# Optimization experiments

Hardware: AMD Instinct MI355X
Metric: run time of the kernel (lower is better)

## Reference

```python
import jax, jax.numpy as jnp
import numpy as np

T, E = 16384, 1024   # frames, feature dim (WavLM-Large)
M, K = 8, 512        # number of kmeans models, clusters per model


def setup_inputs() -> dict:
    key = jax.random.key(0)
    k1, k2, k3 = jax.random.split(key, 3)
    emb = jax.random.normal(k1, (1, T, E), dtype=jnp.float32)
    centroids = jax.random.normal(k2, (M, K, E), dtype=jnp.float32)
    # per-frame random kmeans model choice (stride=1): replaces random.randint in the loop
    model_idx = jax.random.randint(k3, (T,), 0, M, dtype=jnp.int32)
    return {"emb": emb, "centroids": centroids, "model_idx": model_idx}


def reference(emb, centroids, model_idx):
    # emb: [1,T,E], centroids: [M,K,E], model_idx: [T] in [0,M)
    x = emb[0]  # [T,E]
    # squared euclidean distance from every frame to every centroid of every model
    # (argmin over squared dist == argmin over cdist)
    x_sq = jnp.sum(x * x, axis=-1)                      # [T]
    c_sq = jnp.sum(centroids * centroids, axis=-1)      # [M,K]
    dots = jnp.einsum('te,mke->tmk', x, centroids)      # [T,M,K]
    d_all = x_sq[:, None, None] - 2.0 * dots + c_sq[None, :, :]  # [T,M,K]
    # select the randomly chosen model's distances per frame
    d = jnp.take_along_axis(d_all, model_idx[:, None, None].astype(jnp.int32), axis=1)[:, 0, :]  # [T,K]
    codes = jnp.argmin(d, axis=-1)                      # [T]
    # embedding lookup: the quantizer's emb maps cluster id -> centroid vector
    out = centroids[model_idx, codes]                   # [T,E]
    return out[None]  # [1,T,E]
```

## Files before the change

kernel.cpp:

```cpp
#include <hip/hip_runtime.h>


#define T_FRAMES 16384
#define E_DIM    1024
#define M_MODELS 8
#define K_CLUST  512

#define FPB 32
#define NCH 8

typedef __bf16 bf16x8 __attribute__((ext_vector_type(8)));
typedef float  floatx16 __attribute__((ext_vector_type(16)));

__device__ __forceinline__ bf16x8 cvt8(const float4 a, const float4 b) {
  bf16x8 h;
  h[0] = (__bf16)a.x; h[1] = (__bf16)a.y; h[2] = (__bf16)a.z; h[3] = (__bf16)a.w;
  h[4] = (__bf16)b.x; h[5] = (__bf16)b.y; h[6] = (__bf16)b.z; h[7] = (__bf16)b.w;
  return h;
}

__global__ __launch_bounds__(256) void k_cvt(const float* __restrict__ cent,
                                             float* __restrict__ out,
                                             double* __restrict__ csq64) {
  const int b = blockIdx.x;
  const int m = b >> 6;
  const int cg = (b >> 2) & 15;
  const int q = b & 3;
  const int tid = threadIdx.x;
  const int ci = tid & 31;
  const int t8 = tid >> 5;
  const int gk0 = q * 32 + t8 * 4;
  const int B32 = (m * 16 + cg) * 32;
  const float* src = cent + ((size_t)(m * K_CLUST + cg * 32 + ci)) * E_DIM;
  double ss = 0.0;
#pragma unroll
  for (int j = 0; j < 4; ++j) {
    const int gk = gk0 + j;
    const float4 a = *(const float4*)(src + gk * 8);
    const float4 bb = *(const float4*)(src + gk * 8 + 4);
    ss += (double)a.x * a.x + (double)a.y * a.y + (double)a.z * a.z +
          (double)a.w * a.w + (double)bb.x * bb.x + (double)bb.y * bb.y +
          (double)bb.z * bb.z + (double)bb.w * bb.w;
    const size_t foff = (size_t)(B32 + (gk >> 2)) * 1024 + 512 +
                        ((gk & 3) * 32 + ci) * 4;
    *(bf16x8*)(out + foff) = cvt8(a, bb);
  }
  __shared__ double csq_l[32][8];
  csq_l[ci][t8] = ss;
  __syncthreads();
  if (tid < 32) {
    double s = 0.0;
#pragma unroll
    for (int t = 0; t < 8; ++t) s += csq_l[tid][t];
    atomicAdd(&csq64[m * K_CLUST + cg * 32 + tid], s);
  }
}

__global__ __launch_bounds__(256) void k_hist(const int* __restrict__ midx,
                                              int* __restrict__ hist,
                                              double* __restrict__ csq64) {
  __shared__ int h[M_MODELS * 33];
  const int tid = threadIdx.x;
  if (tid < 64) csq64[blockIdx.x * 64 + tid] = 0.0;
  for (int i = tid; i < M_MODELS * 33; i += 256) h[i] = 0;
  __syncthreads();
  const int m = midx[blockIdx.x * 256 + tid];
  atomicAdd(&h[m * 33 + (tid & 31)], 1);
  __syncthreads();
  if (tid < M_MODELS) {
    int s = 0;
    for (int j = 0; j < 32; ++j) s += h[tid * 33 + j];
    hist[blockIdx.x * M_MODELS + tid] = s;
  }
}

__global__ __launch_bounds__(256) void k_scatter(const int* __restrict__ midx,
                                                 const int* __restrict__ hist,
                                                 int* __restrict__ order,
                                                 int* __restrict__ offs) {
  __shared__ int h2[64 * M_MODELS];
  __shared__ int cur[M_MODELS];
  const int tid = threadIdx.x;
  h2[tid] = hist[tid];
  h2[tid + 256] = hist[tid + 256];
  __syncthreads();
  if (tid < M_MODELS) {
    int tot_before = 0;
    for (int mp = 0; mp < tid; ++mp)
      for (int b = 0; b < 64; ++b) tot_before += h2[b * M_MODELS + mp];
    int prior = 0;
    for (int b = 0; b < (int)blockIdx.x; ++b) prior += h2[b * M_MODELS + tid];
    cur[tid] = tot_before + prior;
  }
  if (blockIdx.x == 0 && tid <= M_MODELS) {
    int o = 0;
    for (int mp = 0; mp < tid; ++mp)
      for (int b = 0; b < 64; ++b) o += h2[b * M_MODELS + mp];
    offs[tid] = o;
  }
  __syncthreads();
  const int f = blockIdx.x * 256 + tid;
  const int pos = atomicAdd(&cur[midx[f]], 1);
  order[pos] = f;
}

__global__ __launch_bounds__(512, 4) void k_dist(const float* __restrict__ emb,
                                                 const float* __restrict__ cent,
                                                 const double* __restrict__ csq64,
                                                 const int* __restrict__ order,
                                                 const int* __restrict__ offs,
                                                 float* __restrict__ out) {
  const int m = blockIdx.x;
  const int o0 = offs[m];
  const int cnt = offs[m + 1] - o0;
  const int start = blockIdx.y * FPB;
  if (start >= cnt) return;
  const int nvalid = min(FPB, cnt - start);

  __shared__ __align__(16) __bf16 A_l[2 * 16 * FPB * 8];
  __shared__ int rows_l[FPB];
  __shared__ float wmin_s[8][FPB];
  __shared__ int wcol_s[8][FPB];
  __shared__ float gmin_s[FPB];
  __shared__ int cnt_s[FPB];
  __shared__ int cand_s[FPB][32];

  const int tid = threadIdx.x;
  const int l = tid & 63;
  const int w = tid >> 6;
  const int ln = l & 31;
  const int lh = l >> 5;

  if (tid < FPB) rows_l[tid] = order[o0 + start + min(tid, nvalid - 1)];
  __syncthreads();

  const int s_row = tid & 31;
  const int s_g = tid >> 5;
  const float4* emb4 = (const float4*)emb;
  const size_t arow4 = (size_t)rows_l[s_row] * (E_DIM / 4);

  float4 pa[2];
  pa[0] = emb4[arow4 + s_g * 2 + 0];
  pa[1] = emb4[arow4 + s_g * 2 + 1];
  *(bf16x8*)(A_l + ((s_g)*FPB + s_row) * 8) = cvt8(pa[0], pa[1]);

  const char* bbase[2];
#pragma unroll
  for (int ct = 0; ct < 2; ++ct) {
    const int cg = w * 2 + ct;
    bbase[ct] = (const char*)out + (size_t)(m * 16 + cg) * 131072 + 2048 + l * 16;
  }
#define LOADB(ct, kb) (*(const bf16x8*)(bbase[ct] + (((kb) >> 1) << 12) + (((kb) & 1) << 10)))

  bf16x8 bR[4][2];
#pragma unroll
  for (int d = 0; d < 4; ++d)
#pragma unroll
    for (int ct = 0; ct < 2; ++ct) bR[d][ct] = LOADB(ct, d);

  floatx16 acc[2] = {};

  for (int c = 0; c < NCH; ++c) {
    __syncthreads();
    const int buf = (c & 1) * 16;
    if (c + 1 < NCH) {
      pa[0] = emb4[arow4 + (c + 1) * 32 + s_g * 2 + 0];
      pa[1] = emb4[arow4 + (c + 1) * 32 + s_g * 2 + 1];
    }
#pragma unroll
    for (int jj = 0; jj < 8; ++jj) {
      const int kb = c * 8 + jj;
      const int p = kb & 3;
      const bf16x8 a0 = *(const bf16x8*)(A_l + ((buf + jj * 2 + lh) * FPB + ln) * 8);
      acc[0] = __builtin_amdgcn_mfma_f32_32x32x16_bf16(a0, bR[p][0], acc[0], 0, 0, 0);
      acc[1] = __builtin_amdgcn_mfma_f32_32x32x16_bf16(a0, bR[p][1], acc[1], 0, 0, 0);
      if (kb + 4 < 64) {
        bR[p][0] = LOADB(0, kb + 4);
        bR[p][1] = LOADB(1, kb + 4);
      }
    }
    if (c + 1 < NCH) {
      const int nbuf = ((c + 1) & 1) * 16;
      *(bf16x8*)(A_l + ((nbuf + s_g) * FPB + s_row) * 8) = cvt8(pa[0], pa[1]);
    }
  }
#undef LOADB

  float cs[2];
#pragma unroll
  for (int ct = 0; ct < 2; ++ct)
    cs[ct] = (float)csq64[m * K_CLUST + w * 64 + ct * 32 + ln];

#pragma unroll
  for (int r = 0; r < 16; ++r) {
    const int fr = (r & 3) + 8 * (r >> 2) + 4 * lh;
    float bm = cs[0] - 2.0f * acc[0][r];
    int bc = w * 64 + ln;
    {
      const float s = cs[1] - 2.0f * acc[1][r];
      if (s < bm) { bm = s; bc = w * 64 + 32 + ln; }
    }
#pragma unroll
    for (int sh = 1; sh <= 16; sh <<= 1) {
      const float om = __shfl_xor(bm, sh, 64);
      const int oc = __shfl_xor(bc, sh, 64);
      if (om < bm || (om == bm && oc < bc)) { bm = om; bc = oc; }
    }
    if (ln == 0) { wmin_s[w][fr] = bm; wcol_s[w][fr] = bc; }
  }
  __syncthreads();

  if (tid < FPB) {
    float g = wmin_s[0][tid];
    int gc = wcol_s[0][tid];
#pragma unroll
    for (int w2 = 1; w2 < 8; ++w2) {
      const float v = wmin_s[w2][tid];
      const int vc = wcol_s[w2][tid];
      if (v < g || (v == g && vc < gc)) { g = v; gc = vc; }
    }
    gmin_s[tid] = g;
    cnt_s[tid] = 0;
  }
  __syncthreads();

#pragma unroll
  for (int r = 0; r < 16; ++r) {
    const int fr = (r & 3) + 8 * (r >> 2) + 4 * lh;
    const float thr = gmin_s[fr] + 3.0f;
#pragma unroll
    for (int ct = 0; ct < 2; ++ct) {
      const float s = cs[ct] - 2.0f * acc[ct][r];
      if (s < thr) {
        const int ix = atomicAdd(&cnt_s[fr], 1);
        if (ix < 32) cand_s[fr][ix] = w * 64 + ct * 32 + ln;
      }
    }
  }
  __syncthreads();

  for (int i = 0; i < 4; ++i) {
    const int f = w * 4 + i;
    const int t = rows_l[f];
    const int n = min(cnt_s[f], 32);
    int code;
    if (n == 1) {
      code = cand_s[f][0];
    } else {
      float4 xv[4];
#pragma unroll
      for (int q = 0; q < 4; ++q) xv[q] = emb4[(size_t)t * (E_DIM / 4) + q * 64 + l];
      double bd = 1e300;
      int bi = 1 << 30;
      for (int j = 0; j < n; ++j) {
        const int cc = cand_s[f][j];
        const float4* crow4 = (const float4*)(cent + ((size_t)(m * K_CLUST + cc)) * E_DIM);
        double s = 0.0;
#pragma unroll
        for (int q = 0; q < 4; ++q) {
          const float4 cv = crow4[q * 64 + l];
          s += (double)xv[q].x * cv.x + (double)xv[q].y * cv.y +
               (double)xv[q].z * cv.z + (double)xv[q].w * cv.w;
        }
#pragma unroll
        for (int sh = 32; sh >= 1; sh >>= 1) s += __shfl_xor(s, sh, 64);
        const double d = csq64[m * K_CLUST + cc] - 2.0 * s;
        if (d < bd || (d == bd && cc < bi)) { bd = d; bi = cc; }
      }
      code = bi;
    }
    if (t >= 4096) {
      const float4* crow = (const float4*)(cent + ((size_t)(m * K_CLUST + code)) * E_DIM);
      float4* drow = (float4*)(out + (size_t)t * E_DIM);
#pragma unroll
      for (int q = 0; q < 4; ++q) drow[q * 64 + l] = crow[q * 64 + l];
    } else if (l == 0) {
      *(int*)(out + (size_t)t * E_DIM) = code;
    }
  }
}

__global__ __launch_bounds__(256) void k_gather(const float* __restrict__ cent,
                                                const int* __restrict__ midx,
                                                float* __restrict__ out) {
  const int t = blockIdx.x * 4 + (threadIdx.x >> 6);
  const int l = threadIdx.x & 63;
  float* drow = out + (size_t)t * E_DIM;
  const int code = *(const int*)drow;
  const int m = midx[t];
  const float4* src = (const float4*)(cent + ((size_t)(m * K_CLUST + code)) * E_DIM);
  float4* dst = (float4*)drow;
#pragma unroll
  for (int q = 0; q < 4; ++q) dst[q * 64 + l] = src[q * 64 + l];
}

extern "C" void kernel_launch(void* const* d_in, const int* in_sizes, int n_in,
                              void* d_out, int out_size, void* d_ws, size_t ws_size,
                              hipStream_t stream) {
  const float* emb = (const float*)d_in[0];
  const float* cent = (const float*)d_in[1];
  const int* midx = (const int*)d_in[2];
  float* out = (float*)d_out;

  char* ws = (char*)d_ws;
  double* csq64 = (double*)(ws + 0);
  int* hist = (int*)(ws + 32768);
  int* offs = (int*)(ws + 34816);
  int* order = (int*)(ws + 34880);

  hipLaunchKernelGGL(k_hist, dim3(64), dim3(256), 0, stream, midx, hist, csq64);
  hipLaunchKernelGGL(k_scatter, dim3(64), dim3(256), 0, stream, midx, hist, order, offs);
  hipLaunchKernelGGL(k_cvt, dim3(512), dim3(256), 0, stream, cent, out, csq64);
  hipLaunchKernelGGL(k_dist, dim3(M_MODELS, 80), dim3(512), 0, stream,
                     emb, cent, csq64, order, offs, out);
  hipLaunchKernelGGL(k_gather, dim3(4096 / 4), dim3(256), 0, stream,
                     cent, midx, out);
}
```

Baseline: 202.4 us.

## Double frames per block in distance kernel and move candidate resolve to separate kernel

Raises the distance kernel's frame tile from 32 to 64 rows. Each loaded centroid B fragment now feeds two MFMA row tiles, which halves B traffic per frame, and the grid shrinks accordingly. The fp64 candidate refinement and the centroid copy-out move out of the distance kernel into a new resolve kernel that runs over all frames. The distance kernel now only writes the candidate count and list into the output rows. This trades a lower occupancy bound and an extra global round trip for less B reloading and a lighter tail in the matmul kernel.

```diff
diff --git a/kernel.cpp b/kernel.cpp
--- a/kernel.cpp
+++ b/kernel.cpp
@@ -6,7 +6,7 @@
 #define M_MODELS 8
 #define K_CLUST  512
 
-#define FPB 32
+#define FPB 64
 #define NCH 8
 
 typedef __bf16 bf16x8 __attribute__((ext_vector_type(8)));
@@ -104,7 +104,7 @@
   order[pos] = f;
 }
 
-__global__ __launch_bounds__(512, 4) void k_dist(const float* __restrict__ emb,
+__global__ __launch_bounds__(512, 2) void k_dist(const float* __restrict__ emb,
                                                  const float* __restrict__ cent,
                                                  const double* __restrict__ csq64,
                                                  const int* __restrict__ order,
@@ -134,15 +134,16 @@
   if (tid < FPB) rows_l[tid] = order[o0 + start + min(tid, nvalid - 1)];
   __syncthreads();
 
-  const int s_row = tid & 31;
-  const int s_g = tid >> 5;
+  const int s_row = tid & 63;
+  const int s_g = tid >> 6;
   const float4* emb4 = (const float4*)emb;
   const size_t arow4 = (size_t)rows_l[s_row] * (E_DIM / 4);
 
-  float4 pa[2];
-  pa[0] = emb4[arow4 + s_g * 2 + 0];
-  pa[1] = emb4[arow4 + s_g * 2 + 1];
-  *(bf16x8*)(A_l + ((s_g)*FPB + s_row) * 8) = cvt8(pa[0], pa[1]);
+  float4 pa[4];
+#pragma unroll
+  for (int j = 0; j < 4; ++j) pa[j] = emb4[arow4 + s_g * 4 + j];
+  *(bf16x8*)(A_l + ((s_g * 2 + 0) * FPB + s_row) * 8) = cvt8(pa[0], pa[1]);
+  *(bf16x8*)(A_l + ((s_g * 2 + 1) * FPB + s_row) * 8) = cvt8(pa[2], pa[3]);
 
   const char* bbase[2];
 #pragma unroll
@@ -158,22 +159,25 @@
 #pragma unroll
     for (int ct = 0; ct < 2; ++ct) bR[d][ct] = LOADB(ct, d);
 
-  floatx16 acc[2] = {};
+  floatx16 acc[2][2] = {};
 
   for (int c = 0; c < NCH; ++c) {
     __syncthreads();
     const int buf = (c & 1) * 16;
     if (c + 1 < NCH) {
-      pa[0] = emb4[arow4 + (c + 1) * 32 + s_g * 2 + 0];
-      pa[1] = emb4[arow4 + (c + 1) * 32 + s_g * 2 + 1];
+#pragma unroll
+      for (int j = 0; j < 4; ++j) pa[j] = emb4[arow4 + (c + 1) * 32 + s_g * 4 + j];
     }
 #pragma unroll
     for (int jj = 0; jj < 8; ++jj) {
       const int kb = c * 8 + jj;
       const int p = kb & 3;
       const bf16x8 a0 = *(const bf16x8*)(A_l + ((buf + jj * 2 + lh) * FPB + ln) * 8);
-      acc[0] = __builtin_amdgcn_mfma_f32_32x32x16_bf16(a0, bR[p][0], acc[0], 0, 0, 0);
-      acc[1] = __builtin_amdgcn_mfma_f32_32x32x16_bf16(a0, bR[p][1], acc[1], 0, 0, 0);
+      const bf16x8 a1 = *(const bf16x8*)(A_l + ((buf + jj * 2 + lh) * FPB + 32 + ln) * 8);
+      acc[0][0] = __builtin_amdgcn_mfma_f32_32x32x16_bf16(a0, bR[p][0], acc[0][0], 0, 0, 0);
+      acc[0][1] = __builtin_amdgcn_mfma_f32_32x32x16_bf16(a0, bR[p][1], acc[0][1], 0, 0, 0);
+      acc[1][0] = __builtin_amdgcn_mfma_f32_32x32x16_bf16(a1, bR[p][0], acc[1][0], 0, 0, 0);
+      acc[1][1] = __builtin_amdgcn_mfma_f32_32x32x16_bf16(a1, bR[p][1], acc[1][1], 0, 0, 0);
       if (kb + 4 < 64) {
         bR[p][0] = LOADB(0, kb + 4);
         bR[p][1] = LOADB(1, kb + 4);
@@ -181,7 +185,8 @@
     }
     if (c + 1 < NCH) {
       const int nbuf = ((c + 1) & 1) * 16;
-      *(bf16x8*)(A_l + ((nbuf + s_g) * FPB + s_row) * 8) = cvt8(pa[0], pa[1]);
+      *(bf16x8*)(A_l + ((nbuf + s_g * 2 + 0) * FPB + s_row) * 8) = cvt8(pa[0], pa[1]);
+      *(bf16x8*)(A_l + ((nbuf + s_g * 2 + 1) * FPB + s_row) * 8) = cvt8(pa[2], pa[3]);
     }
   }
 #undef LOADB
@@ -192,102 +197,106 @@
     cs[ct] = (float)csq64[m * K_CLUST + w * 64 + ct * 32 + ln];
 
 #pragma unroll
-  for (int r = 0; r < 16; ++r) {
-    const int fr = (r & 3) + 8 * (r >> 2) + 4 * lh;
-    float bm = cs[0] - 2.0f * acc[0][r];
-    int bc = w * 64 + ln;
-    {
-      const float s = cs[1] - 2.0f * acc[1][r];
-      if (s < bm) { bm = s; bc = w * 64 + 32 + ln; }
-    }
-#pragma unroll
-    for (int sh = 1; sh <= 16; sh <<= 1) {
-      const float om = __shfl_xor(bm, sh, 64);
-      const int oc = __shfl_xor(bc, sh, 64);
-      if (om < bm || (om == bm && oc < bc)) { bm = om; bc = oc; }
-    }
-    if (ln == 0) { wmin_s[w][fr] = bm; wcol_s[w][fr] = bc; }
-  }
-  __syncthreads();
-
-  if (tid < FPB) {
-    float g = wmin_s[0][tid];
-    int gc = wcol_s[0][tid];
+  for (int rt = 0; rt < 2; ++rt) {
+#pragma unroll
+    for (int r = 0; r < 16; ++r) {
+      const int fr = rt * 32 + (r & 3) + 8 * (r >> 2) + 4 * lh;
+      float bm = cs[0] - 2.0f * acc[rt][0][r];
+      int bc = w * 64 + ln;
+      {
+        const float s = cs[1] - 2.0f * acc[rt][1][r];
+        if (s < bm) { bm = s; bc = w * 64 + 32 + ln; }
+      }
+#pragma unroll
+      for (int sh = 1; sh <= 16; sh <<= 1) {
+        const float om = __shfl_xor(bm, sh, 64);
+        const int oc = __shfl_xor(bc, sh, 64);
+        if (om < bm || (om == bm && oc < bc)) { bm = om; bc = oc; }
+      }
+      if (ln == 0) { wmin_s[w][fr] = bm; wcol_s[w][fr] = bc; }
+    }
+  }
+  __syncthreads();
+
+  for (int f0 = tid; f0 < FPB; f0 += 512) {
+    float g = wmin_s[0][f0];
+    int gc = wcol_s[0][f0];
 #pragma unroll
     for (int w2 = 1; w2 < 8; ++w2) {
-      const float v = wmin_s[w2][tid];
-      const int vc = wcol_s[w2][tid];
+      const float v = wmin_s[w2][f0];
+      const int vc = wcol_s[w2][f0];
       if (v < g || (v == g && vc < gc)) { g = v; gc = vc; }
     }
-    gmin_s[tid] = g;
-    cnt_s[tid] = 0;
-  }
-  __syncthreads();
-
-#pragma unroll
-  for (int r = 0; r < 16; ++r) {
-    const int fr = (r & 3) + 8 * (r >> 2) + 4 * lh;
-    const float thr = gmin_s[fr] + 3.0f;
-#pragma unroll
-    for (int ct = 0; ct < 2; ++ct) {
-      const float s = cs[ct] - 2.0f * acc[ct][r];
-      if (s < thr) {
-        const int ix = atomicAdd(&cnt_s[fr], 1);
-        if (ix < 32) cand_s[fr][ix] = w * 64 + ct * 32 + ln;
-      }
-    }
-  }
-  __syncthreads();
-
-  for (int i = 0; i < 4; ++i) {
-    const int f = w * 4 + i;
+    gmin_s[f0] = g;
+    cnt_s[f0] = 0;
+  }
+  __syncthreads();
+
+#pragma unroll
+  for (int rt = 0; rt < 2; ++rt) {
+#pragma unroll
+    for (int r = 0; r < 16; ++r) {
+      const int fr = rt * 32 + (r & 3) + 8 * (r >> 2) + 4 * lh;
+      const float thr = gmin_s[fr] + 3.0f;
+#pragma unroll
+      for (int ct = 0; ct < 2; ++ct) {
+        const float s = cs[ct] - 2.0f * acc[rt][ct][r];
+        if (s < thr) {
+          const int ix = atomicAdd(&cnt_s[fr], 1);
+          if (ix < 32) cand_s[fr][ix] = w * 64 + ct * 32 + ln;
+        }
+      }
+    }
+  }
+  __syncthreads();
+
+  for (int i = 0; i < 8; ++i) {
+    const int f = w * 8 + i;
+    if (f >= nvalid) continue;
     const int t = rows_l[f];
     const int n = min(cnt_s[f], 32);
-    int code;
-    if (n == 1) {
-      code = cand_s[f][0];
-    } else {
-      float4 xv[4];
-#pragma unroll
-      for (int q = 0; q < 4; ++q) xv[q] = emb4[(size_t)t * (E_DIM / 4) + q * 64 + l];
-      double bd = 1e300;
-      int bi = 1 << 30;
-      for (int j = 0; j < n; ++j) {
-        const int cc = cand_s[f][j];
-        const float4* crow4 = (const float4*)(cent + ((size_t)(m * K_CLUST + cc)) * E_DIM);
-        double s = 0.0;
-#pragma unroll
-        for (int q = 0; q < 4; ++q) {
-          const float4 cv = crow4[q * 64 + l];
-          s += (double)xv[q].x * cv.x + (double)xv[q].y * cv.y +
-               (double)xv[q].z * cv.z + (double)xv[q].w * cv.w;
-        }
-#pragma unroll
-        for (int sh = 32; sh >= 1; sh >>= 1) s += __shfl_xor(s, sh, 64);
-        const double d = csq64[m * K_CLUST + cc] - 2.0 * s;
-        if (d < bd || (d == bd && cc < bi)) { bd = d; bi = cc; }
-      }
-      code = bi;
-    }
-    if (t >= 4096) {
-      const float4* crow = (const float4*)(cent + ((size_t)(m * K_CLUST + code)) * E_DIM);
-      float4* drow = (float4*)(out + (size_t)t * E_DIM);
-#pragma unroll
-      for (int q = 0; q < 4; ++q) drow[q * 64 + l] = crow[q * 64 + l];
-    } else if (l == 0) {
-      *(int*)(out + (size_t)t * E_DIM) = code;
-    }
-  }
-}
-
-__global__ __launch_bounds__(256) void k_gather(const float* __restrict__ cent,
-                                                const int* __restrict__ midx,
-                                                float* __restrict__ out) {
+    if (l == 0) *(int*)(out + (size_t)t * E_DIM) = n;
+    else if (l <= n) *(int*)(out + (size_t)t * E_DIM + l) = cand_s[f][l - 1];
+  }
+}
+
+__global__ __launch_bounds__(256) void k_resolve(const float* __restrict__ emb,
+                                                 const float* __restrict__ cent,
+                                                 const double* __restrict__ csq64,
+                                                 const int* __restrict__ midx,
+                                                 float* __restrict__ out) {
   const int t = blockIdx.x * 4 + (threadIdx.x >> 6);
   const int l = threadIdx.x & 63;
+  const int m = midx[t];
   float* drow = out + (size_t)t * E_DIM;
-  const int code = *(const int*)drow;
-  const int m = midx[t];
+  const int n = *(const int*)drow;
+  int code;
+  if (n == 1) {
+    code = *(const int*)(drow + 1);
+  } else {
+    const float4* emb4 = (const float4*)emb;
+    float4 xv[4];
+#pragma unroll
+    for (int q = 0; q < 4; ++q) xv[q] = emb4[(size_t)t * (E_DIM / 4) + q * 64 + l];
+    double bd = 1e300;
+    int bi = 1 << 30;
+    for (int j = 0; j < n; ++j) {
+      const int cc = *(const int*)(drow + 1 + j);
+      const float4* crow4 = (const float4*)(cent + ((size_t)(m * K_CLUST + cc)) * E_DIM);
+      double s = 0.0;
+#pragma unroll
+      for (int q = 0; q < 4; ++q) {
+        const float4 cv = crow4[q * 64 + l];
+        s += (double)xv[q].x * cv.x + (double)xv[q].y * cv.y +
+             (double)xv[q].z * cv.z + (double)xv[q].w * cv.w;
+      }
+#pragma unroll
+      for (int sh = 32; sh >= 1; sh >>= 1) s += __shfl_xor(s, sh, 64);
+      const double d = csq64[m * K_CLUST + cc] - 2.0 * s;
+      if (d < bd || (d == bd && cc < bi)) { bd = d; bi = cc; }
+    }
+    code = bi;
+  }
   const float4* src = (const float4*)(cent + ((size_t)(m * K_CLUST + code)) * E_DIM);
   float4* dst = (float4*)drow;
 #pragma unroll
@@ -311,8 +320,8 @@
   hipLaunchKernelGGL(k_hist, dim3(64), dim3(256), 0, stream, midx, hist, csq64);
   hipLaunchKernelGGL(k_scatter, dim3(64), dim3(256), 0, stream, midx, hist, order, offs);
   hipLaunchKernelGGL(k_cvt, dim3(512), dim3(256), 0, stream, cent, out, csq64);
-  hipLaunchKernelGGL(k_dist, dim3(M_MODELS, 80), dim3(512), 0, stream,
+  hipLaunchKernelGGL(k_dist, dim3(M_MODELS, 40), dim3(512), 0, stream,
                      emb, cent, csq64, order, offs, out);
-  hipLaunchKernelGGL(k_gather, dim3(4096 / 4), dim3(256), 0, stream,
-                     cent, midx, out);
-}
+  hipLaunchKernelGGL(k_resolve, dim3(T_FRAMES / 4), dim3(256), 0, stream,
+                     emb, cent, csq64, midx, out);
+}
```

Result: slower. 210.1 us (+3.8%).
